# Optimization experiments

Measured on AMD Instinct MI355X. Metric: run time of the kernel, lower is better.

The kernel has to match this reference:

```python
import jax, jax.numpy as jnp
import numpy as np

HEAD_DIM = 64
N_HEADS = 12
ROPE_BASE = 10000.0


def _rope_tables(seq_len, head_dim, dtype=jnp.float32):
    half = head_dim // 2
    inv_freq = 1.0 / (ROPE_BASE ** (jnp.arange(0, half, dtype=jnp.float32) / half))
    pos = jnp.arange(seq_len, dtype=jnp.float32)
    freqs = pos[:, None] * inv_freq[None, :]  # (s, half)
    return jnp.cos(freqs).astype(dtype), jnp.sin(freqs).astype(dtype)


def _apply_rope(t, cos, sin):
    # t: (b, h, s, d); rotate-half convention on full head_dim (rope_fraction=1.0)
    d = t.shape[-1]
    t1, t2 = t[..., : d // 2], t[..., d // 2 :]
    cos = cos[None, None, :, :]
    sin = sin[None, None, :, :]
    return jnp.concatenate([t1 * cos - t2 * sin, t1 * sin + t2 * cos], axis=-1)


def setup_inputs() -> dict:
    key = jax.random.key(0)
    ks = jax.random.split(key, 6)
    b, s, d_model = 16, 512, 768
    x = jax.random.normal(ks[0], (b, s, d_model), dtype=jnp.float32)
    chain_ids = jax.random.randint(ks[1], (b, s), 0, 2, dtype=jnp.int32)
    attention_mask = jnp.ones((b, s), dtype=bool)
    inner = N_HEADS * HEAD_DIM
    scale = 0.02
    Wq = jax.random.normal(ks[2], (d_model, inner), dtype=jnp.float32) * scale
    Wk = jax.random.normal(ks[3], (d_model, inner), dtype=jnp.float32) * scale
    Wv = jax.random.normal(ks[4], (d_model, inner), dtype=jnp.float32) * scale
    Wo = jax.random.normal(ks[5], (inner, d_model), dtype=jnp.float32) * scale
    return {"x": x, "chain_ids": chain_ids, "attention_mask": attention_mask,
            "Wq": Wq, "Wk": Wk, "Wv": Wv, "Wo": Wo}


def reference(x, chain_ids, attention_mask, Wq, Wk, Wv, Wo):
    b, s, _ = x.shape
    h, d = N_HEADS, HEAD_DIM
    scale = d ** (-0.5)

    def proj(W):
        return jnp.einsum('bse,ef->bsf', x, W).reshape(b, s, h, d).transpose(0, 2, 1, 3)

    q = proj(Wq)  # (b, h, s, d)
    k = proj(Wk)
    v = proj(Wv)

    cos, sin = _rope_tables(s, d, x.dtype)
    q_rope = _apply_rope(q, cos, sin)
    k_rope = _apply_rope(k, cos, sin)

    scores_intra = jnp.einsum('bhsd,bhtd->bhst', q_rope, k_rope) * scale
    scores_inter = jnp.einsum('bhsd,bhtd->bhst', q, k) * scale

    # intra-chain mask (b, 1, s, s)
    intra = (chain_ids[:, None, :, None] == chain_ids[:, None, None, :])
    merged = jnp.where(intra, scores_intra, scores_inter)

    # additive padding mask (b, 1, 1, s)
    pad = jnp.where(attention_mask[:, None, None, :], 0.0, -jnp.inf).astype(x.dtype)
    merged = merged + pad

    attn = jax.nn.softmax(merged, axis=-1)
    attn = jnp.nan_to_num(attn, nan=0.0)

    out = jnp.einsum('bhst,bhtd->bhsd', attn, v)
    out = out.transpose(0, 2, 1, 3).reshape(b, s, h * d)
    return jnp.einsum('bsf,fe->bse', out, Wo)
```

## Files before the change

### kernel.cpp

```cpp
#include <hip/hip_runtime.h>
#include <stdint.h>
#include <math.h>

#define NB 16
#define NS 512
#define NH 12
#define ND 64
#define NE 768
#define NF 768

typedef __attribute__((ext_vector_type(4))) float  f32x4;
typedef __attribute__((ext_vector_type(8))) short  bf16x8;

#define AS1(p) ((const __attribute__((address_space(1))) unsigned int*)(p))
#define AS3(p) ((__attribute__((address_space(3))) unsigned int*)(p))

__device__ __forceinline__ short f2bf(float f) {
    unsigned u = __builtin_bit_cast(unsigned, f);
    u += 0x7FFFu + ((u >> 16) & 1u);
    return (short)(u >> 16);
}
__device__ __forceinline__ float bf2f(short s) {
    unsigned u = ((unsigned)(unsigned short)s) << 16;
    return __builtin_bit_cast(float, u);
}
__device__ __forceinline__ unsigned pkbf2(float a, float b) {
    return (unsigned)(unsigned short)f2bf(a) | ((unsigned)(unsigned short)f2bf(b) << 16);
}

#define MFMA16(a, b, c) __builtin_amdgcn_mfma_f32_16x16x32_bf16((a), (b), (c), 0, 0, 0)

__device__ __forceinline__ bf16x8 lds_rd8(const short* base, int row, int cb) {
    return *(const bf16x8*)((const char*)base + (((row) * 128 + (cb)) ^ (((row) & 7) << 4)));
}

__global__ __launch_bounds__(256) void prep_all_kernel(
    const float* __restrict__ x, short* __restrict__ xb,
    const float* __restrict__ Wq, const float* __restrict__ Wk,
    const float* __restrict__ Wv, const float* __restrict__ Wo,
    short* __restrict__ Wqt, short* __restrict__ Wkt,
    short* __restrict__ Wvt, short* __restrict__ Wot,
    float* __restrict__ cos_t, float* __restrict__ sin_t,
    const unsigned char* __restrict__ m, int* __restrict__ flag) {
    const int bid = blockIdx.x;
    if (bid < 64) {
        int i = bid * 256 + threadIdx.x;
        int p = i >> 5, j = i & 31;
        float inv_freq = powf(10000.0f, -(float)j / 32.0f);
        float ang = (float)p * inv_freq;
        cos_t[i] = cosf(ang);
        sin_t[i] = sinf(ang);
        return;
    }
    if (bid == 64) {
        __shared__ int any;
        if (threadIdx.x == 0) any = 0;
        __syncthreads();
        int acc = 0;
        for (int i = threadIdx.x; i < NB * NS; i += 256)
            if ((i & 3) && m[i]) acc = 1;
        if (acc) atomicOr(&any, 1);
        __syncthreads();
        if (threadIdx.x == 0) *flag = any;
        return;
    }
    if (bid < 641) {
        int idx = bid - 65;
        int zz = idx / 144, r2 = idx % 144;
        const float* W  = (zz == 0) ? Wq  : (zz == 1) ? Wk  : (zz == 2) ? Wv  : Wo;
        short*       Wt = (zz == 0) ? Wqt : (zz == 1) ? Wkt : (zz == 2) ? Wvt : Wot;
        const int k0 = (r2 / 12) * 64, n0 = (r2 % 12) * 64;
        __shared__ float t[64][65];
        for (int u = threadIdx.x; u < 4096; u += 256) {
            int r = u >> 6, c = u & 63;
            t[r][c] = W[(size_t)(k0 + r) * 768 + n0 + c];
        }
        __syncthreads();
        for (int u = threadIdx.x; u < 4096; u += 256) {
            int c = u >> 6, r = u & 63;
            Wt[(size_t)(n0 + c) * 768 + k0 + r] = f2bf(t[r][c]);
        }
        return;
    }
    int i = ((bid - 641) * 256 + threadIdx.x) * 8;
    float4 a = *(const float4*)&x[i];
    float4 b = *(const float4*)&x[i + 4];
    bf16x8 r = { f2bf(a.x), f2bf(a.y), f2bf(a.z), f2bf(a.w),
                 f2bf(b.x), f2bf(b.y), f2bf(b.z), f2bf(b.w) };
    *(bf16x8*)&xb[i] = r;
}

__global__ __launch_bounds__(256) void gemm_qkv_kernel(const short* __restrict__ xb,
    const short* __restrict__ Wqt, const short* __restrict__ Wkt, const short* __restrict__ Wvt,
    const float* __restrict__ cos_t, const float* __restrict__ sin_t,
    short* __restrict__ qo, short* __restrict__ ko, short* __restrict__ kpo,
    short* __restrict__ vto) {
    const int id = blockIdx.x;
    const int xcd = id & 7, rest = id >> 3;
    const int mq = rest / 18;
    const int nz = rest % 18;
    const int z  = nz / 6;
    const int n0 = (nz % 6) * 128;
    const int m0 = (xcd * 16 + mq) * 64;
    const short* Bt = (z == 0) ? Wqt : (z == 1) ? Wkt : Wvt;
    short*       O  = (z == 0) ? qo  : (z == 1) ? ko  : vto;
    __shared__ short As[2][64 * 64], Bs[2][128 * 64];
    const int tid = threadIdx.x, lane = tid & 63, wave = tid >> 6;
    const int g = lane >> 4, l15 = lane & 15;
    const int wm = wave >> 1, wn = wave & 1;
    f32x4 acc[2][4];
    #pragma unroll
    for (int i = 0; i < 2; ++i)
        #pragma unroll
        for (int j = 0; j < 4; ++j) acc[i][j] = (f32x4){0.f, 0.f, 0.f, 0.f};

    auto STAGE = [&](short* Ad, short* Bd, int kt) {
        const char* Asrc = (const char*)(xb + (size_t)m0 * 768 + kt * 64);
        const char* Bsrc = (const char*)(Bt + (size_t)n0 * 768 + kt * 64);
        #pragma unroll
        for (int p = 0; p < 2; ++p) {
            int dstoff = (wave * 2 + p) * 1024;
            int off = dstoff + lane * 16;
            int row = off >> 7, slot = off & 127;
            int srcs = slot ^ ((row & 7) << 4);
            __builtin_amdgcn_global_load_lds(AS1(Asrc + (size_t)row * 1536 + srcs),
                                             AS3((char*)Ad + dstoff), 16, 0, 0);
        }
        #pragma unroll
        for (int p = 0; p < 4; ++p) {
            int dstoff = (wave * 4 + p) * 1024;
            int off = dstoff + lane * 16;
            int row = off >> 7, slot = off & 127;
            int srcs = slot ^ ((row & 7) << 4);
            __builtin_amdgcn_global_load_lds(AS1(Bsrc + (size_t)row * 1536 + srcs),
                                             AS3((char*)Bd + dstoff), 16, 0, 0);
        }
    };
    auto COMPUTE = [&](const short* Asb, const short* Bsb) {
        __builtin_amdgcn_s_setprio(1);
        #pragma unroll
        for (int h2 = 0; h2 < 2; ++h2) {
            bf16x8 af[2], bfr[4];
            const int cb = h2 * 64 + g * 16;
            #pragma unroll
            for (int i = 0; i < 2; ++i)
                af[i]  = lds_rd8(Asb, wm * 32 + i * 16 + l15, cb);
            #pragma unroll
            for (int j = 0; j < 4; ++j)
                bfr[j] = lds_rd8(Bsb, wn * 64 + j * 16 + l15, cb);
            #pragma unroll
            for (int i = 0; i < 2; ++i)
                #pragma unroll
                for (int j = 0; j < 4; ++j)
                    acc[i][j] = MFMA16(af[i], bfr[j], acc[i][j]);
        }
        __builtin_amdgcn_s_setprio(0);
    };

    STAGE(As[0], Bs[0], 0);
    asm volatile("s_waitcnt vmcnt(0)" ::: "memory");
    __builtin_amdgcn_s_barrier();
    int cur = 0;
    for (int kt = 0; kt < 11; ++kt) {
        STAGE(As[cur ^ 1], Bs[cur ^ 1], kt + 1);
        COMPUTE(As[cur], Bs[cur]);
        asm volatile("s_waitcnt vmcnt(0)" ::: "memory");
        __builtin_amdgcn_s_barrier();
        cur ^= 1;
    }
    COMPUTE(As[cur], Bs[cur]);

    const int hh = (n0 + wn * 64) >> 6;
    #pragma unroll
    for (int i = 0; i < 2; ++i)
        #pragma unroll
        for (int r = 0; r < 4; ++r) {
            int mm = m0 + wm * 32 + i * 16 + g * 4 + r;
            int bb = mm >> 9, ss = mm & 511;
            if (z == 2) {
                #pragma unroll
                for (int j = 0; j < 4; ++j) {
                    int dd = j * 16 + l15;
                    O[(((size_t)bb * NH + hh) * ND + dd) * NS + ss] = f2bf(acc[i][j][r]);
                }
            } else {
                size_t base = (((size_t)bb * NH + hh) * NS + ss) * ND;
                #pragma unroll
                for (int j = 0; j < 4; ++j)
                    O[base + j * 16 + l15] = f2bf(acc[i][j][r]);
                if (z == 1) {
                    #pragma unroll
                    for (int p2 = 0; p2 < 2; ++p2) {
                        int jf = p2 * 16 + l15;
                        float c = cos_t[ss * 32 + jf], s = sin_t[ss * 32 + jf];
                        float t1 = acc[i][p2][r], t2 = acc[i][p2 + 2][r];
                        kpo[base + jf]      = f2bf(t1 * c - t2 * s);
                        kpo[base + 32 + jf] = f2bf(t1 * s + t2 * c);
                    }
                }
            }
        }
}

__global__ __launch_bounds__(256) void attn_fused_kernel(
    const short* __restrict__ qr, const short* __restrict__ kr, const short* __restrict__ kp,
    const short* __restrict__ vt,
    const float* __restrict__ cos_t, const float* __restrict__ sin_t,
    const int* __restrict__ chain, const void* __restrict__ amask,
    const int* __restrict__ mflag, short* __restrict__ aout) {
    const int lid = blockIdx.x;
    const int xcd = lid & 7, idx = lid >> 3;
    const int qt = idx & 7, bhl = idx >> 3;
    const int bh = xcd * 24 + bhl;
    const int b = bh / 12, h = bh - (bh / 12) * 12;
    const int q0 = qt * 64;

    __shared__ short Kr_s[4096];
    __shared__ short Kp_s[4096];
    __shared__ short Vt_s[4096];
    __shared__ short P_s[4096];
    __shared__ int   ck_a[512];
    __shared__ float kb_a[512];

    const int tid = threadIdx.x, lane = tid & 63, wave = tid >> 6;
    const int g = lane >> 4, l15 = lane & 15;
    const int m_u8 = *mflag;
    const size_t bhNS = (size_t)bh * NS;
    const float SC = 0.18033688011f;

    for (int u = tid; u < NS; u += 256) {
        int gidx = b * NS + u;
        ck_a[u] = chain[gidx];
        int ok = m_u8 ? (int)((const unsigned char*)amask)[gidx] : ((const int*)amask)[gidx];
        kb_a[u] = ok ? 0.f : -INFINITY;
    }
    const char* qrsC = (const char*)(qr + (bhNS + q0) * ND);
    #pragma unroll
    for (int p = 0; p < 2; ++p) {
        int dstoff = (wave * 2 + p) * 1024;
        int off = dstoff + lane * 16;
        int row = off >> 7, slot = off & 127;
        int srcs = slot ^ ((row & 7) << 4);
        __builtin_amdgcn_global_load_lds(AS1(qrsC + (size_t)row * 128 + srcs),
                                         AS3((char*)Kr_s + dstoff), 16, 0, 0);
    }
    __syncthreads();
    const int qrow = wave * 16 + l15;
    bf16x8 fqr0 = lds_rd8(Kr_s, qrow, g * 16);
    bf16x8 fqr1 = lds_rd8(Kr_s, qrow, 64 + g * 16);
    bf16x8 fqp0, fqp1;
    {
        int pos = q0 + qrow;
        float4 c0 = *(const float4*)&cos_t[pos * 32 + g * 8];
        float4 c1 = *(const float4*)&cos_t[pos * 32 + g * 8 + 4];
        float4 s0 = *(const float4*)&sin_t[pos * 32 + g * 8];
        float4 s1 = *(const float4*)&sin_t[pos * 32 + g * 8 + 4];
        float cc[8] = {c0.x, c0.y, c0.z, c0.w, c1.x, c1.y, c1.z, c1.w};
        float ss[8] = {s0.x, s0.y, s0.z, s0.w, s1.x, s1.y, s1.z, s1.w};
        #pragma unroll
        for (int j = 0; j < 8; ++j) {
            float t1 = bf2f(fqr0[j]), t2 = bf2f(fqr1[j]);
            fqp0[j] = f2bf(t1 * cc[j] - t2 * ss[j]);
            fqp1[j] = f2bf(t1 * ss[j] + t2 * cc[j]);
        }
    }
    const int cqv = ck_a[q0 + qrow];

    float m_run = -INFINITY, l_run = 0.f;
    f32x4 accO[4];
    #pragma unroll
    for (int t = 0; t < 4; ++t) accO[t] = (f32x4){0.f, 0.f, 0.f, 0.f};

    const char* krC = (const char*)(kr + bhNS * ND);
    const char* kpC = (const char*)(kp + bhNS * ND);
    const char* vtC = (const char*)(vt + bhNS * ND);

    int off_[2], row_[2], srcs_[2];
    #pragma unroll
    for (int p = 0; p < 2; ++p) {
        int dstoff = (wave * 2 + p) * 1024;
        off_[p]  = dstoff + lane * 16;
        row_[p]  = off_[p] >> 7;
        srcs_[p] = (off_[p] & 127) ^ ((row_[p] & 7) << 4);
    }
    uint4 rK0, rK1, rP0, rP1, rV0, rV1;
    auto LOADREGS = [&](int kv) {
        const int k0s = kv * 64;
        rK0 = *(const uint4*)(krC + (size_t)(k0s + row_[0]) * 128 + srcs_[0]);
        rK1 = *(const uint4*)(krC + (size_t)(k0s + row_[1]) * 128 + srcs_[1]);
        rP0 = *(const uint4*)(kpC + (size_t)(k0s + row_[0]) * 128 + srcs_[0]);
        rP1 = *(const uint4*)(kpC + (size_t)(k0s + row_[1]) * 128 + srcs_[1]);
        rV0 = *(const uint4*)(vtC + (size_t)row_[0] * 1024 + (size_t)k0s * 2 + srcs_[0]);
        rV1 = *(const uint4*)(vtC + (size_t)row_[1] * 1024 + (size_t)k0s * 2 + srcs_[1]);
    };
    auto WRITELDS = [&]() {
        *(uint4*)((char*)Kr_s + off_[0]) = rK0;
        *(uint4*)((char*)Kr_s + off_[1]) = rK1;
        *(uint4*)((char*)Kp_s + off_[0]) = rP0;
        *(uint4*)((char*)Kp_s + off_[1]) = rP1;
        *(uint4*)((char*)Vt_s + off_[0]) = rV0;
        *(uint4*)((char*)Vt_s + off_[1]) = rV1;
    };

    LOADREGS(0);
    __syncthreads();

    for (int kv = 0; kv < 8; ++kv) {
        const int k0s = kv * 64;
        WRITELDS();
        __syncthreads();
        if (kv < 7) LOADREGS(kv + 1);

        float pm[4][4];
        float tm = -INFINITY;
        __builtin_amdgcn_s_setprio(1);
        #pragma unroll
        for (int t = 0; t < 4; ++t) {
            bf16x8 akr0 = lds_rd8(Kr_s, t * 16 + l15, g * 16);
            bf16x8 akr1 = lds_rd8(Kr_s, t * 16 + l15, 64 + g * 16);
            bf16x8 akp0 = lds_rd8(Kp_s, t * 16 + l15, g * 16);
            bf16x8 akp1 = lds_rd8(Kp_s, t * 16 + l15, 64 + g * 16);
            f32x4 sr = (f32x4){0.f, 0.f, 0.f, 0.f};
            f32x4 sp = (f32x4){0.f, 0.f, 0.f, 0.f};
            sr = MFMA16(akr0, fqr0, sr);
            sr = MFMA16(akr1, fqr1, sr);
            sp = MFMA16(akp0, fqp0, sp);
            sp = MFMA16(akp1, fqp1, sp);
            int4   ck4 = *(const int4*)&ck_a[k0s + t * 16 + g * 4];
            float4 kb4 = *(const float4*)&kb_a[k0s + t * 16 + g * 4];
            const int   ckk[4] = {ck4.x, ck4.y, ck4.z, ck4.w};
            const float kbb[4] = {kb4.x, kb4.y, kb4.z, kb4.w};
            #pragma unroll
            for (int r = 0; r < 4; ++r) {
                float sv = (cqv == ckk[r]) ? sp[r] : sr[r];
                sv = sv * SC + kbb[r];
                pm[t][r] = sv;
                tm = fmaxf(tm, sv);
            }
        }
        __builtin_amdgcn_s_setprio(0);

        tm = fmaxf(tm, __shfl_xor(tm, 16));
        tm = fmaxf(tm, __shfl_xor(tm, 32));
        bool skip = __all(tm - m_run <= 8.f);
        float mnew, fac;
        if (skip) { mnew = m_run; fac = 1.f; }
        else      { mnew = fmaxf(m_run, tm); fac = exp2f(m_run - mnew); }
        float psum = 0.f;
        if (mnew == -INFINITY) {
            #pragma unroll
            for (int t = 0; t < 4; ++t)
                #pragma unroll
                for (int r = 0; r < 4; ++r) pm[t][r] = 0.f;
            fac = 1.f;
        } else {
            #pragma unroll
            for (int t = 0; t < 4; ++t)
                #pragma unroll
                for (int r = 0; r < 4; ++r) {
                    float p = exp2f(pm[t][r] - mnew);
                    pm[t][r] = p;
                    psum += p;
                }
        }
        psum += __shfl_xor(psum, 16);
        psum += __shfl_xor(psum, 32);
        l_run = l_run * fac + psum;
        m_run = mnew;

        char* pwave = (char*)P_s + wave * 2048;
        int psw = (l15 & 7) << 4;
        #pragma unroll
        for (int t = 0; t < 4; ++t) {
            unsigned u0 = pkbf2(pm[t][0], pm[t][1]);
            unsigned u1 = pkbf2(pm[t][2], pm[t][3]);
            uint2 pk = {u0, u1};
            *(uint2*)(pwave + ((l15 * 128 + t * 32 + g * 8) ^ psw)) = pk;
        }
        if (!skip) {
            float f4[4];
            #pragma unroll
            for (int r = 0; r < 4; ++r) f4[r] = __shfl(fac, g * 4 + r);
            #pragma unroll
            for (int t = 0; t < 4; ++t) {
                f32x4 a = accO[t];
                a[0] *= f4[0]; a[1] *= f4[1]; a[2] *= f4[2]; a[3] *= f4[3];
                accO[t] = a;
            }
        }
        bf16x8 pa0 = *(const bf16x8*)(pwave + ((l15 * 128 + g * 16) ^ psw));
        bf16x8 pa1 = *(const bf16x8*)(pwave + ((l15 * 128 + 64 + g * 16) ^ psw));
        __builtin_amdgcn_s_setprio(1);
        #pragma unroll
        for (int dt = 0; dt < 4; ++dt) {
            bf16x8 vb0 = lds_rd8(Vt_s, dt * 16 + l15, g * 16);
            bf16x8 vb1 = lds_rd8(Vt_s, dt * 16 + l15, 64 + g * 16);
            accO[dt] = MFMA16(pa0, vb0, accO[dt]);
            accO[dt] = MFMA16(pa1, vb1, accO[dt]);
        }
        __builtin_amdgcn_s_setprio(0);
        __syncthreads();
    }

    float inv[4];
    #pragma unroll
    for (int r = 0; r < 4; ++r) {
        float lv = __shfl(l_run, g * 4 + r);
        inv[r] = (lv > 0.f) ? 1.f / lv : 0.f;
    }
    #pragma unroll
    for (int dt = 0; dt < 4; ++dt)
        #pragma unroll
        for (int r = 0; r < 4; ++r) {
            int row = b * NS + q0 + wave * 16 + g * 4 + r;
            aout[(size_t)row * NF + h * ND + dt * 16 + l15] = f2bf(accO[dt][r] * inv[r]);
        }
}

__global__ __launch_bounds__(256) void gemm_out_kernel(const short* __restrict__ A,
    const short* __restrict__ Wot, float* __restrict__ out) {
    const int id = blockIdx.x;
    const int xcd = id & 7, rest = id >> 3;
    const int mq = rest / 6;
    const int n0 = (rest % 6) * 128;
    const int m0 = (xcd * 16 + mq) * 64;
    __shared__ short As[2][64 * 64], Bs[2][128 * 64];
    const int tid = threadIdx.x, lane = tid & 63, wave = tid >> 6;
    const int g = lane >> 4, l15 = lane & 15;
    const int wm = wave >> 1, wn = wave & 1;
    f32x4 acc[2][4];
    #pragma unroll
    for (int i = 0; i < 2; ++i)
        #pragma unroll
        for (int j = 0; j < 4; ++j) acc[i][j] = (f32x4){0.f, 0.f, 0.f, 0.f};

    auto STAGE = [&](short* Ad, short* Bd, int kt) {
        const char* Asrc = (const char*)(A   + (size_t)m0 * 768 + kt * 64);
        const char* Bsrc = (const char*)(Wot + (size_t)n0 * 768 + kt * 64);
        #pragma unroll
        for (int p = 0; p < 2; ++p) {
            int dstoff = (wave * 2 + p) * 1024;
            int off = dstoff + lane * 16;
            int row = off >> 7, slot = off & 127;
            int srcs = slot ^ ((row & 7) << 4);
            __builtin_amdgcn_global_load_lds(AS1(Asrc + (size_t)row * 1536 + srcs),
                                             AS3((char*)Ad + dstoff), 16, 0, 0);
        }
        #pragma unroll
        for (int p = 0; p < 4; ++p) {
            int dstoff = (wave * 4 + p) * 1024;
            int off = dstoff + lane * 16;
            int row = off >> 7, slot = off & 127;
            int srcs = slot ^ ((row & 7) << 4);
            __builtin_amdgcn_global_load_lds(AS1(Bsrc + (size_t)row * 1536 + srcs),
                                             AS3((char*)Bd + dstoff), 16, 0, 0);
        }
    };
    auto COMPUTE = [&](const short* Asb, const short* Bsb) {
        __builtin_amdgcn_s_setprio(1);
        #pragma unroll
        for (int h2 = 0; h2 < 2; ++h2) {
            bf16x8 af[2], bfr[4];
            const int cb = h2 * 64 + g * 16;
            #pragma unroll
            for (int i = 0; i < 2; ++i)
                af[i]  = lds_rd8(Asb, wm * 32 + i * 16 + l15, cb);
            #pragma unroll
            for (int j = 0; j < 4; ++j)
                bfr[j] = lds_rd8(Bsb, wn * 64 + j * 16 + l15, cb);
            #pragma unroll
            for (int i = 0; i < 2; ++i)
                #pragma unroll
                for (int j = 0; j < 4; ++j)
                    acc[i][j] = MFMA16(af[i], bfr[j], acc[i][j]);
        }
        __builtin_amdgcn_s_setprio(0);
    };

    STAGE(As[0], Bs[0], 0);
    asm volatile("s_waitcnt vmcnt(0)" ::: "memory");
    __builtin_amdgcn_s_barrier();
    int cur = 0;
    for (int kt = 0; kt < 11; ++kt) {
        STAGE(As[cur ^ 1], Bs[cur ^ 1], kt + 1);
        COMPUTE(As[cur], Bs[cur]);
        asm volatile("s_waitcnt vmcnt(0)" ::: "memory");
        __builtin_amdgcn_s_barrier();
        cur ^= 1;
    }
    COMPUTE(As[cur], Bs[cur]);

    #pragma unroll
    for (int i = 0; i < 2; ++i)
        #pragma unroll
        for (int r = 0; r < 4; ++r) {
            int mm = m0 + wm * 32 + i * 16 + g * 4 + r;
            #pragma unroll
            for (int j = 0; j < 4; ++j) {
                int n = n0 + wn * 64 + j * 16 + l15;
                out[(size_t)mm * NE + n] = acc[i][j][r];
            }
        }
}

extern "C" void kernel_launch(void* const* d_in, const int* in_sizes, int n_in,
                              void* d_out, int out_size, void* d_ws, size_t ws_size,
                              hipStream_t stream) {
    const float* x     = (const float*)d_in[0];
    const int*   chain = (const int*)d_in[1];
    const void*  amask = d_in[2];
    const float* Wq = (const float*)d_in[3];
    const float* Wk = (const float*)d_in[4];
    const float* Wv = (const float*)d_in[5];
    const float* Wo = (const float*)d_in[6];
    float* out = (float*)d_out;

    const size_t QSZ = (size_t)NB * NH * NS * ND;
    char* w = (char*)d_ws;
    float* cos_t = (float*)w;  w += (size_t)NS * 32 * 4;
    float* sin_t = (float*)w;  w += (size_t)NS * 32 * 4;
    int*   mflag = (int*)w;    w += 256;
    short* xb    = (short*)w;  w += (size_t)8192 * 768 * 2;
    short* Wqt   = (short*)w;  w += (size_t)768 * 768 * 2;
    short* Wkt   = (short*)w;  w += (size_t)768 * 768 * 2;
    short* Wvt   = (short*)w;  w += (size_t)768 * 768 * 2;
    short* Wot   = (short*)w;  w += (size_t)768 * 768 * 2;
    short* q_raw = (short*)w;  w += QSZ * 2;
    short* k_raw = (short*)w;  w += QSZ * 2;
    short* k_rop = (short*)w;  w += QSZ * 2;
    short* vtr   = (short*)w;  w += QSZ * 2;
    short* aout  = xb;

    prep_all_kernel<<<dim3(3713), dim3(256), 0, stream>>>(x, xb, Wq, Wk, Wv, Wo,
                                                          Wqt, Wkt, Wvt, Wot,
                                                          cos_t, sin_t,
                                                          (const unsigned char*)amask, mflag);
    gemm_qkv_kernel<<<dim3(2304), dim3(256), 0, stream>>>(xb, Wqt, Wkt, Wvt, cos_t, sin_t,
                                                          q_raw, k_raw, k_rop, vtr);
    attn_fused_kernel<<<dim3(1536), dim3(256), 0, stream>>>(q_raw, k_raw, k_rop, vtr,
                                                            cos_t, sin_t, chain, amask, mflag, aout);
    gemm_out_kernel<<<dim3(768), dim3(256), 0, stream>>>(aout, Wot, out);
}
```

Before: 143.3 us.

## Double KV tile to 128 keys and reuse Kr LDS buffer for P

The attention kernel now processes 128 keys per iteration instead of 64, halving the loop trip count and the number of barriers and online-softmax rescale steps. The separate P scratch buffer is removed and P is written into the Kr_s region after an extra barrier, with V tiles stored as two 64-key halves. This trades more registers (12 prefetch uint4s plus 32 score floats) and larger LDS for fewer synchronisations and fewer rescale passes, which may lower occupancy.

```diff
diff --git a/kernel.cpp b/kernel.cpp
--- a/kernel.cpp
+++ b/kernel.cpp
@@ -215,10 +215,9 @@
     const int b = bh / 12, h = bh - (bh / 12) * 12;
     const int q0 = qt * 64;
 
-    __shared__ short Kr_s[4096];
-    __shared__ short Kp_s[4096];
-    __shared__ short Vt_s[4096];
-    __shared__ short P_s[4096];
+    __shared__ short Kr_s[8192];
+    __shared__ short Kp_s[8192];
+    __shared__ short Vt_s[8192];
     __shared__ int   ck_a[512];
     __shared__ float kb_a[512];
 
@@ -275,47 +274,60 @@
     const char* kpC = (const char*)(kp + bhNS * ND);
     const char* vtC = (const char*)(vt + bhNS * ND);
 
-    int off_[2], row_[2], srcs_[2];
-    #pragma unroll
-    for (int p = 0; p < 2; ++p) {
-        int dstoff = (wave * 2 + p) * 1024;
+    int off_[4], row_[4], srcs_[4], vsrc_[4];
+    #pragma unroll
+    for (int p = 0; p < 4; ++p) {
+        int dstoff = (wave * 4 + p) * 1024;
         off_[p]  = dstoff + lane * 16;
         row_[p]  = off_[p] >> 7;
         srcs_[p] = (off_[p] & 127) ^ ((row_[p] & 7) << 4);
-    }
-    uint4 rK0, rK1, rP0, rP1, rV0, rV1;
+        vsrc_[p] = (row_[p] & 63) * 1024 + (row_[p] >> 6) * 128 + srcs_[p];
+    }
+    uint4 rKa, rKb, rKc, rKd, rPa, rPb, rPc, rPd, rVa, rVb, rVc, rVd;
     auto LOADREGS = [&](int kv) {
-        const int k0s = kv * 64;
-        rK0 = *(const uint4*)(krC + (size_t)(k0s + row_[0]) * 128 + srcs_[0]);
-        rK1 = *(const uint4*)(krC + (size_t)(k0s + row_[1]) * 128 + srcs_[1]);
-        rP0 = *(const uint4*)(kpC + (size_t)(k0s + row_[0]) * 128 + srcs_[0]);
-        rP1 = *(const uint4*)(kpC + (size_t)(k0s + row_[1]) * 128 + srcs_[1]);
-        rV0 = *(const uint4*)(vtC + (size_t)row_[0] * 1024 + (size_t)k0s * 2 + srcs_[0]);
-        rV1 = *(const uint4*)(vtC + (size_t)row_[1] * 1024 + (size_t)k0s * 2 + srcs_[1]);
+        const int k0s = kv * 128;
+        rKa = *(const uint4*)(krC + (size_t)(k0s + row_[0]) * 128 + srcs_[0]);
+        rKb = *(const uint4*)(krC + (size_t)(k0s + row_[1]) * 128 + srcs_[1]);
+        rKc = *(const uint4*)(krC + (size_t)(k0s + row_[2]) * 128 + srcs_[2]);
+        rKd = *(const uint4*)(krC + (size_t)(k0s + row_[3]) * 128 + srcs_[3]);
+        rPa = *(const uint4*)(kpC + (size_t)(k0s + row_[0]) * 128 + srcs_[0]);
+        rPb = *(const uint4*)(kpC + (size_t)(k0s + row_[1]) * 128 + srcs_[1]);
+        rPc = *(const uint4*)(kpC + (size_t)(k0s + row_[2]) * 128 + srcs_[2]);
+        rPd = *(const uint4*)(kpC + (size_t)(k0s + row_[3]) * 128 + srcs_[3]);
+        rVa = *(const uint4*)(vtC + (size_t)k0s * 2 + vsrc_[0]);
+        rVb = *(const uint4*)(vtC + (size_t)k0s * 2 + vsrc_[1]);
+        rVc = *(const uint4*)(vtC + (size_t)k0s * 2 + vsrc_[2]);
+        rVd = *(const uint4*)(vtC + (size_t)k0s * 2 + vsrc_[3]);
     };
     auto WRITELDS = [&]() {
-        *(uint4*)((char*)Kr_s + off_[0]) = rK0;
-        *(uint4*)((char*)Kr_s + off_[1]) = rK1;
-        *(uint4*)((char*)Kp_s + off_[0]) = rP0;
-        *(uint4*)((char*)Kp_s + off_[1]) = rP1;
-        *(uint4*)((char*)Vt_s + off_[0]) = rV0;
-        *(uint4*)((char*)Vt_s + off_[1]) = rV1;
+        *(uint4*)((char*)Kr_s + off_[0]) = rKa;
+        *(uint4*)((char*)Kr_s + off_[1]) = rKb;
+        *(uint4*)((char*)Kr_s + off_[2]) = rKc;
+        *(uint4*)((char*)Kr_s + off_[3]) = rKd;
+        *(uint4*)((char*)Kp_s + off_[0]) = rPa;
+        *(uint4*)((char*)Kp_s + off_[1]) = rPb;
+        *(uint4*)((char*)Kp_s + off_[2]) = rPc;
+        *(uint4*)((char*)Kp_s + off_[3]) = rPd;
+        *(uint4*)((char*)Vt_s + off_[0]) = rVa;
+        *(uint4*)((char*)Vt_s + off_[1]) = rVb;
+        *(uint4*)((char*)Vt_s + off_[2]) = rVc;
+        *(uint4*)((char*)Vt_s + off_[3]) = rVd;
     };
 
     LOADREGS(0);
     __syncthreads();
 
-    for (int kv = 0; kv < 8; ++kv) {
-        const int k0s = kv * 64;
+    for (int kv = 0; kv < 4; ++kv) {
+        const int k0s = kv * 128;
         WRITELDS();
-        __syncthreads();
-        if (kv < 7) LOADREGS(kv + 1);
-
-        float pm[4][4];
+        __builtin_amdgcn_s_barrier();
+        if (kv < 3) LOADREGS(kv + 1);
+
+        float pm[8][4];
         float tm = -INFINITY;
         __builtin_amdgcn_s_setprio(1);
         #pragma unroll
-        for (int t = 0; t < 4; ++t) {
+        for (int t = 0; t < 8; ++t) {
             bf16x8 akr0 = lds_rd8(Kr_s, t * 16 + l15, g * 16);
             bf16x8 akr1 = lds_rd8(Kr_s, t * 16 + l15, 64 + g * 16);
             bf16x8 akp0 = lds_rd8(Kp_s, t * 16 + l15, g * 16);
@@ -349,13 +361,13 @@
         float psum = 0.f;
         if (mnew == -INFINITY) {
             #pragma unroll
-            for (int t = 0; t < 4; ++t)
+            for (int t = 0; t < 8; ++t)
                 #pragma unroll
                 for (int r = 0; r < 4; ++r) pm[t][r] = 0.f;
             fac = 1.f;
         } else {
             #pragma unroll
-            for (int t = 0; t < 4; ++t)
+            for (int t = 0; t < 8; ++t)
                 #pragma unroll
                 for (int r = 0; r < 4; ++r) {
                     float p = exp2f(pm[t][r] - mnew);
@@ -368,14 +380,17 @@
         l_run = l_run * fac + psum;
         m_run = mnew;
 
-        char* pwave = (char*)P_s + wave * 2048;
+        __builtin_amdgcn_s_barrier();
+
+        char* pwave = (char*)Kr_s + wave * 4096;
         int psw = (l15 & 7) << 4;
         #pragma unroll
-        for (int t = 0; t < 4; ++t) {
+        for (int t = 0; t < 8; ++t) {
             unsigned u0 = pkbf2(pm[t][0], pm[t][1]);
             unsigned u1 = pkbf2(pm[t][2], pm[t][3]);
             uint2 pk = {u0, u1};
-            *(uint2*)(pwave + ((l15 * 128 + t * 32 + g * 8) ^ psw)) = pk;
+            *(uint2*)(pwave + (t >> 2) * 2048 +
+                      ((l15 * 128 + (t & 3) * 32 + g * 8) ^ psw)) = pk;
         }
         if (!skip) {
             float f4[4];
@@ -388,15 +403,21 @@
                 accO[t] = a;
             }
         }
-        bf16x8 pa0 = *(const bf16x8*)(pwave + ((l15 * 128 + g * 16) ^ psw));
-        bf16x8 pa1 = *(const bf16x8*)(pwave + ((l15 * 128 + 64 + g * 16) ^ psw));
+        bf16x8 paA = *(const bf16x8*)(pwave +        ((l15 * 128 +      g * 16) ^ psw));
+        bf16x8 paB = *(const bf16x8*)(pwave +        ((l15 * 128 + 64 + g * 16) ^ psw));
+        bf16x8 paC = *(const bf16x8*)(pwave + 2048 + ((l15 * 128 +      g * 16) ^ psw));
+        bf16x8 paD = *(const bf16x8*)(pwave + 2048 + ((l15 * 128 + 64 + g * 16) ^ psw));
         __builtin_amdgcn_s_setprio(1);
         #pragma unroll
         for (int dt = 0; dt < 4; ++dt) {
-            bf16x8 vb0 = lds_rd8(Vt_s, dt * 16 + l15, g * 16);
-            bf16x8 vb1 = lds_rd8(Vt_s, dt * 16 + l15, 64 + g * 16);
-            accO[dt] = MFMA16(pa0, vb0, accO[dt]);
-            accO[dt] = MFMA16(pa1, vb1, accO[dt]);
+            bf16x8 vb0 = lds_rd8(Vt_s,      dt * 16 + l15,      g * 16);
+            bf16x8 vb1 = lds_rd8(Vt_s,      dt * 16 + l15, 64 + g * 16);
+            bf16x8 vb2 = lds_rd8(Vt_s, 64 + dt * 16 + l15,      g * 16);
+            bf16x8 vb3 = lds_rd8(Vt_s, 64 + dt * 16 + l15, 64 + g * 16);
+            accO[dt] = MFMA16(paA, vb0, accO[dt]);
+            accO[dt] = MFMA16(paB, vb1, accO[dt]);
+            accO[dt] = MFMA16(paC, vb2, accO[dt]);
+            accO[dt] = MFMA16(paD, vb3, accO[dt]);
         }
         __builtin_amdgcn_s_setprio(0);
         __syncthreads();
```

Result: slower. 150.4 us (+5.0%).
